# Kernel tuning notes

Measured on AMD Instinct MI355X. Metric: run time of the kernel, lower is better.

Reference implementation:

```python
import jax, jax.numpy as jnp
import numpy as np

TOP_K = 16
NUM_HEADS = 1
EPS = 1e-8  # torch F.cosine_similarity eps


def setup_inputs() -> dict:
    key = jax.random.key(0)
    ks = jax.random.split(key, 8)
    B, N, Dk, Dv = 64, 8192, 256, 256
    return {
        "query": jax.random.normal(ks[0], (B, Dk), jnp.float32),
        "key_memory": jax.random.normal(ks[1], (B, N, Dk), jnp.float32),
        "value_memory": jax.random.normal(ks[2], (B, N, Dv), jnp.float32),
        "iteration": jax.random.randint(ks[3], (B, 1), 0, N),
        "in_proj_w": jax.random.normal(ks[4], (3 * Dv, Dv), jnp.float32) * 0.06,
        "in_proj_b": jnp.zeros((3 * Dv,), jnp.float32),
        "out_proj_w": jax.random.normal(ks[5], (Dv, Dv), jnp.float32) * 0.06,
        "out_proj_b": jnp.zeros((Dv,), jnp.float32),
    }


def _mha(x, in_w, in_b, out_w, out_b):
    # torch nn.MultiheadAttention (batch_first, qkv same embed dim) self-attention
    B, T, E = x.shape
    H = NUM_HEADS
    hd = E // H
    qkv = x @ in_w.T + in_b                      # [B,T,3E]
    q, k, v = jnp.split(qkv, 3, axis=-1)

    def heads(t):
        return t.reshape(B, T, H, hd).transpose(0, 2, 1, 3)  # [B,H,T,hd]

    q, k, v = heads(q), heads(k), heads(v)
    scale = jnp.asarray(1.0 / np.sqrt(hd), x.dtype)
    attn = jax.nn.softmax(jnp.einsum('bhqd,bhkd->bhqk', q, k) * scale, axis=-1)
    o = jnp.einsum('bhqk,bhkd->bhqd', attn, v).transpose(0, 2, 1, 3).reshape(B, T, E)
    return o @ out_w.T + out_b


def reference(query, key_memory, value_memory, iteration,
              in_proj_w, in_proj_b, out_proj_w, out_proj_b):
    B, N, Dv = value_memory.shape
    # memory validity mask: item n is valid iff n <= iteration[b]
    mem_idx = jnp.arange(N)[None, :]                                   # [1,N]
    mask = (mem_idx <= iteration).astype(key_memory.dtype)[..., None]  # [B,N,1]
    km = key_memory * mask
    vm = value_memory * mask

    # masked cosine similarity between each memory key and the query
    num = jnp.einsum('bnd,bd->bn', km, query)                          # [B,N]
    denom = jnp.maximum(
        jnp.linalg.norm(km, axis=-1) * jnp.linalg.norm(query, axis=-1, keepdims=True),
        EPS)
    sim = num / denom                                                  # [B,N]

    topk_sim, topk_idx = jax.lax.top_k(sim, TOP_K)                     # [B,K]
    topk_vm = jnp.take_along_axis(vm, topk_idx[:, :, None], axis=1)    # [B,K,Dv]

    wv = jax.nn.softmax(topk_sim, axis=-1)[..., None]                  # [B,K,1]
    nrv = wv * topk_vm                                                 # [B,K,Dv]

    nrv = _mha(nrv, in_proj_w, in_proj_b, out_proj_w, out_proj_b)      # [B,K,Dv]

    # rows with iteration == 0 are left as zeros (scatter of computed rows)
    not_first = (iteration.reshape(-1) > 0).astype(nrv.dtype)[:, None, None]
    nrv = nrv * not_first
    return nrv.sum(axis=1)                                             # [B,Dv]
```

## Files before the change

kernel.cpp:

```cpp
#include <hip/hip_runtime.h>
#include <hip/hip_bf16.h>
#include <math.h>

#define B_   64
#define N_   8192
#define D_   256
#define K_   16
#define NCH_ 32
#define CPB_ 2048
#define EPS_ 1e-8f
#define NEG_ -3.4e38f

static const size_t CANDV_OFF = 0;
static const size_t CANDI_OFF = 131072;
static const size_t QKV_OFF   = 262144;

__global__ void __launch_bounds__(256)
simtopk_kernel(const float* __restrict__ q, const float* __restrict__ km,
               const int* __restrict__ iter,
               float* __restrict__ cand_v, int* __restrict__ cand_i) {
    int b     = blockIdx.x >> 5;
    int chunk = blockIdx.x & (NCH_ - 1);
    int tid   = threadIdx.x;
    int w     = tid >> 6;
    int lane  = tid & 63;
    int g     = lane >> 4;
    int p     = lane & 15;
    int it    = iter[b];
    int r0    = (chunk << 8) + (w << 6);
    size_t cbase = ((size_t)blockIdx.x * 4 + w) * K_;

    if (r0 > it) {
        if (lane < K_) { cand_v[cbase + lane] = 0.f; cand_i[cbase + lane] = r0 + lane; }
        return;
    }

    __shared__ float svals[256];

    float4 q4[4];
    #pragma unroll
    for (int k = 0; k < 4; k++)
        q4[k] = *(const float4*)(q + (size_t)b * D_ + k * 64 + p * 4);
    float qq = 0.f;
    #pragma unroll
    for (int k = 0; k < 4; k++)
        qq += q4[k].x*q4[k].x + q4[k].y*q4[k].y + q4[k].z*q4[k].z + q4[k].w*q4[k].w;
    #pragma unroll
    for (int off = 8; off; off >>= 1) qq += __shfl_xor(qq, off);
    float qn = sqrtf(qq);

    for (int t = 0; t < 16; t++) {
        int r = r0 + (t << 2) + g;
        float s = 0.f;
        if (r <= it) {
            const float* rp = km + ((size_t)b * N_ + r) * D_;
            float dot = 0.f, sq = 0.f;
            #pragma unroll
            for (int k = 0; k < 4; k++) {
                float4 kv = *(const float4*)(rp + k * 64 + p * 4);
                dot += kv.x*q4[k].x + kv.y*q4[k].y + kv.z*q4[k].z + kv.w*q4[k].w;
                sq  += kv.x*kv.x + kv.y*kv.y + kv.z*kv.z + kv.w*kv.w;
            }
            #pragma unroll
            for (int off = 8; off; off >>= 1) {
                dot += __shfl_xor(dot, off);
                sq  += __shfl_xor(sq,  off);
            }
            s = dot / fmaxf(sqrtf(sq) * qn, EPS_);
        }
        if (p == 0) svals[(w << 6) + (t << 2) + g] = s;
    }

    float v  = svals[(w << 6) + lane];
    int  idx = r0 + lane;
    for (int sel = 0; sel < K_; sel++) {
        float bv = v; int bi = idx;
        #pragma unroll
        for (int off = 32; off; off >>= 1) {
            float ov = __shfl_xor(bv, off);
            int   oi = __shfl_xor(bi, off);
            if (ov > bv || (ov == bv && oi < bi)) { bv = ov; bi = oi; }
        }
        if (idx == bi) v = NEG_;
        if (lane == 0) { cand_v[cbase + sel] = bv; cand_i[cbase + sel] = bi; }
    }
}

__global__ void __launch_bounds__(256)
merge_qkv_kernel(const float* __restrict__ cand_v, const int* __restrict__ cand_i,
                 const float* __restrict__ vm, const int* __restrict__ iter,
                 const float* __restrict__ inw, const float* __restrict__ inb,
                 float* __restrict__ qkv) {
    int b = blockIdx.x / 3, which = blockIdx.x - b * 3;
    int tid = threadIdx.x, w = tid >> 6, lane = tid & 63;
    int it = iter[b];
    if (it == 0) return;

    float cv[8]; int ci[8];
    #pragma unroll
    for (int j = 0; j < 8; j++) {
        cv[j] = cand_v[(size_t)b * CPB_ + (j << 8) + tid];
        ci[j] = cand_i[(size_t)b * CPB_ + (j << 8) + tid];
    }

    __shared__ float rv4[4]; __shared__ int ri4[4];
    __shared__ float selv[K_]; __shared__ int seli[K_];
    __shared__ float w16[K_];
    __shared__ float xs[D_][K_];

    for (int sel = 0; sel < K_; sel++) {
        float bv = cv[0]; int bi = ci[0];
        #pragma unroll
        for (int j = 1; j < 8; j++)
            if (cv[j] > bv || (cv[j] == bv && ci[j] < bi)) { bv = cv[j]; bi = ci[j]; }
        #pragma unroll
        for (int off = 32; off; off >>= 1) {
            float ov = __shfl_xor(bv, off);
            int   oi = __shfl_xor(bi, off);
            if (ov > bv || (ov == bv && oi < bi)) { bv = ov; bi = oi; }
        }
        if (lane == 0) { rv4[w] = bv; ri4[w] = bi; }
        __syncthreads();
        float wv = rv4[0]; int wi = ri4[0];
        #pragma unroll
        for (int w2 = 1; w2 < 4; w2++)
            if (rv4[w2] > wv || (rv4[w2] == wv && ri4[w2] < wi)) { wv = rv4[w2]; wi = ri4[w2]; }
        #pragma unroll
        for (int j = 0; j < 8; j++) if (ci[j] == wi) cv[j] = NEG_;
        if (tid == 0) { selv[sel] = wv; seli[sel] = wi; }
        __syncthreads();
    }

    if (tid < K_) {
        float m = NEG_;
        for (int jj = 0; jj < K_; jj++) m = fmaxf(m, selv[jj]);
        float ssum = 0.f;
        for (int jj = 0; jj < K_; jj++) ssum += expf(selv[jj] - m);
        w16[tid] = expf(selv[tid] - m) / ssum;
    }
    __syncthreads();

    #pragma unroll
    for (int k = 0; k < K_; k++) {
        int row = seli[k];
        float val = (row <= it) ? w16[k] * vm[((size_t)b * N_ + row) * D_ + tid] : 0.f;
        xs[tid][k] = val;
    }
    __syncthreads();

    float acc[K_];
    #pragma unroll
    for (int k = 0; k < K_; k++) acc[k] = 0.f;
    const float* wrow = inw + ((size_t)(which * D_ + tid)) * D_;
    for (int d = 0; d < D_; d += 4) {
        float4 wv4 = *(const float4*)(wrow + d);
        float wk[4] = {wv4.x, wv4.y, wv4.z, wv4.w};
        #pragma unroll
        for (int dd = 0; dd < 4; dd++) {
            float wgt = wk[dd];
            float4 x0 = *(const float4*)(&xs[d + dd][0]);
            float4 x1 = *(const float4*)(&xs[d + dd][4]);
            float4 x2 = *(const float4*)(&xs[d + dd][8]);
            float4 x3 = *(const float4*)(&xs[d + dd][12]);
            acc[0]  += x0.x * wgt; acc[1]  += x0.y * wgt; acc[2]  += x0.z * wgt; acc[3]  += x0.w * wgt;
            acc[4]  += x1.x * wgt; acc[5]  += x1.y * wgt; acc[6]  += x1.z * wgt; acc[7]  += x1.w * wgt;
            acc[8]  += x2.x * wgt; acc[9]  += x2.y * wgt; acc[10] += x2.z * wgt; acc[11] += x2.w * wgt;
            acc[12] += x3.x * wgt; acc[13] += x3.y * wgt; acc[14] += x3.z * wgt; acc[15] += x3.w * wgt;
        }
    }
    float bias = inb[which * D_ + tid];
    #pragma unroll
    for (int k = 0; k < K_; k++)
        qkv[(((size_t)b * 3 + which) * K_ + k) * D_ + tid] = acc[k] + bias;
}

__global__ void __launch_bounds__(256)
final_kernel(const float* __restrict__ qkv, const int* __restrict__ iter,
             const float* __restrict__ ow, const float* __restrict__ ob,
             float* __restrict__ out) {
    int b = blockIdx.x, tid = threadIdx.x;
    int it = iter[b];
    if (it == 0) { out[(size_t)b * D_ + tid] = 0.f; return; }
    __shared__ float qs[K_][D_ + 1];
    __shared__ float ks[K_][D_ + 1];
    __shared__ float vs[K_][D_ + 1];
    __shared__ float attn[K_][K_];
    __shared__ float colsum[K_];
    __shared__ float so[D_];
    const float* base = qkv + (size_t)b * 3 * K_ * D_;
    #pragma unroll
    for (int k = 0; k < K_; k++) {
        qs[k][tid] = base[(0 * K_ + k) * D_ + tid];
        ks[k][tid] = base[(1 * K_ + k) * D_ + tid];
        vs[k][tid] = base[(2 * K_ + k) * D_ + tid];
    }
    __syncthreads();
    int i = tid >> 4, j = tid & 15;
    float s = 0.f;
    for (int d = 0; d < D_; d++) s += qs[i][d] * ks[j][d];
    attn[i][j] = s * 0.0625f;
    __syncthreads();
    if (tid < K_) {
        float m = NEG_;
        for (int jj = 0; jj < K_; jj++) m = fmaxf(m, attn[tid][jj]);
        float ssum = 0.f;
        for (int jj = 0; jj < K_; jj++) ssum += expf(attn[tid][jj] - m);
        float inv = 1.f / ssum;
        for (int jj = 0; jj < K_; jj++) attn[tid][jj] = expf(attn[tid][jj] - m) * inv;
    }
    __syncthreads();
    if (tid < K_) {
        float c = 0.f;
        for (int ii = 0; ii < K_; ii++) c += attn[ii][tid];
        colsum[tid] = c;
    }
    __syncthreads();
    float acc = 0.f;
    #pragma unroll
    for (int jj = 0; jj < K_; jj++) acc += colsum[jj] * vs[jj][tid];
    so[tid] = acc;
    __syncthreads();
    float o = 0.f;
    const float* orow = ow + (size_t)tid * D_;
    for (int e = 0; e < D_; e += 4) {
        float4 wv = *(const float4*)(orow + e);
        float4 sv = *(const float4*)(&so[e]);
        o += sv.x * wv.x + sv.y * wv.y + sv.z * wv.z + sv.w * wv.w;
    }
    out[(size_t)b * D_ + tid] = o + 16.f * ob[tid];
}

extern "C" void kernel_launch(void* const* d_in, const int* in_sizes, int n_in,
                              void* d_out, int out_size, void* d_ws, size_t ws_size,
                              hipStream_t stream) {
    const float* q   = (const float*)d_in[0];
    const float* km  = (const float*)d_in[1];
    const float* vm  = (const float*)d_in[2];
    const int*   it  = (const int*)  d_in[3];
    const float* inw = (const float*)d_in[4];
    const float* inb = (const float*)d_in[5];
    const float* ow  = (const float*)d_in[6];
    const float* ob  = (const float*)d_in[7];
    float* out = (float*)d_out;

    float* ws     = (float*)d_ws;
    float* cand_v = ws + CANDV_OFF;
    int*   cand_i = (int*)(ws + CANDI_OFF);
    float* qkv    = ws + QKV_OFF;

    simtopk_kernel<<<dim3(B_ * NCH_), dim3(256), 0, stream>>>(q, km, it, cand_v, cand_i);
    merge_qkv_kernel<<<dim3(B_ * 3), dim3(256), 0, stream>>>(cand_v, cand_i, vm, it, inw, inb, qkv);
    final_kernel<<<dim3(B_), dim3(256), 0, stream>>>(qkv, it, ow, ob, out);
}
```

Measured before the change: 128.6 us.

## Rework similarity top-k with bitonic sort and streamlined merge/projection kernels

The similarity kernel now has each wavefront handle two rows per step with clamped, branch-free loads, which adds memory-level parallelism. The 16 iterative argmax passes are replaced by a full 64-lane bitonic sort. The merge kernel does the 2048-candidate selection in a single wavefront without block barriers, folds the softmax weight into a per-row scale applied after projection, and reads value rows directly from global memory with weights held in registers, instead of staging through shared memory. The attention kernel pads its shared rows and uses float4 reads. The trade-off is that one-wave selection serializes more work, and value rows are re-read per block.

```diff
diff --git a/kernel.cpp b/kernel.cpp
--- a/kernel.cpp
+++ b/kernel.cpp
@@ -6,8 +6,6 @@
 #define N_   8192
 #define D_   256
 #define K_   16
-#define NCH_ 32
-#define CPB_ 2048
 #define EPS_ 1e-8f
 #define NEG_ -3.4e38f
 
@@ -19,71 +17,91 @@
 simtopk_kernel(const float* __restrict__ q, const float* __restrict__ km,
                const int* __restrict__ iter,
                float* __restrict__ cand_v, int* __restrict__ cand_i) {
-    int b     = blockIdx.x >> 5;
-    int chunk = blockIdx.x & (NCH_ - 1);
-    int tid   = threadIdx.x;
-    int w     = tid >> 6;
-    int lane  = tid & 63;
-    int g     = lane >> 4;
-    int p     = lane & 15;
-    int it    = iter[b];
-    int r0    = (chunk << 8) + (w << 6);
-    size_t cbase = ((size_t)blockIdx.x * 4 + w) * K_;
+    int tid  = threadIdx.x;
+    int w    = tid >> 6, lane = tid & 63;
+    int g    = lane >> 4, p = lane & 15;
+    int item = (blockIdx.x << 2) + w;
+    int b    = item >> 7;
+    int r0   = (item & 127) << 6;
+    int it   = iter[b];
+    size_t cbase = (size_t)item * K_;
 
     if (r0 > it) {
         if (lane < K_) { cand_v[cbase + lane] = 0.f; cand_i[cbase + lane] = r0 + lane; }
         return;
     }
 
-    __shared__ float svals[256];
-
     float4 q4[4];
     #pragma unroll
-    for (int k = 0; k < 4; k++)
-        q4[k] = *(const float4*)(q + (size_t)b * D_ + k * 64 + p * 4);
+    for (int kk = 0; kk < 4; kk++)
+        q4[kk] = *(const float4*)(q + (size_t)b * D_ + kk * 64 + p * 4);
     float qq = 0.f;
     #pragma unroll
-    for (int k = 0; k < 4; k++)
-        qq += q4[k].x*q4[k].x + q4[k].y*q4[k].y + q4[k].z*q4[k].z + q4[k].w*q4[k].w;
+    for (int kk = 0; kk < 4; kk++)
+        qq += q4[kk].x*q4[kk].x + q4[kk].y*q4[kk].y + q4[kk].z*q4[kk].z + q4[kk].w*q4[kk].w;
     #pragma unroll
     for (int off = 8; off; off >>= 1) qq += __shfl_xor(qq, off);
     float qn = sqrtf(qq);
 
-    for (int t = 0; t < 16; t++) {
-        int r = r0 + (t << 2) + g;
-        float s = 0.f;
-        if (r <= it) {
-            const float* rp = km + ((size_t)b * N_ + r) * D_;
-            float dot = 0.f, sq = 0.f;
-            #pragma unroll
-            for (int k = 0; k < 4; k++) {
-                float4 kv = *(const float4*)(rp + k * 64 + p * 4);
-                dot += kv.x*q4[k].x + kv.y*q4[k].y + kv.z*q4[k].z + kv.w*q4[k].w;
-                sq  += kv.x*kv.x + kv.y*kv.y + kv.z*kv.z + kv.w*kv.w;
-            }
-            #pragma unroll
-            for (int off = 8; off; off >>= 1) {
-                dot += __shfl_xor(dot, off);
-                sq  += __shfl_xor(sq,  off);
-            }
-            s = dot / fmaxf(sqrtf(sq) * qn, EPS_);
-        }
-        if (p == 0) svals[(w << 6) + (t << 2) + g] = s;
-    }
-
-    float v  = svals[(w << 6) + lane];
-    int  idx = r0 + lane;
-    for (int sel = 0; sel < K_; sel++) {
-        float bv = v; int bi = idx;
-        #pragma unroll
-        for (int off = 32; off; off >>= 1) {
-            float ov = __shfl_xor(bv, off);
-            int   oi = __shfl_xor(bi, off);
-            if (ov > bv || (ov == bv && oi < bi)) { bv = ov; bi = oi; }
-        }
-        if (idx == bi) v = NEG_;
-        if (lane == 0) { cand_v[cbase + sel] = bv; cand_i[cbase + sel] = bi; }
-    }
+    float keepv = 0.f;
+    const float* kmb = km + (size_t)b * N_ * D_;
+    for (int t = 0; t < 8; t++) {
+        int ra = r0 + (t << 3) + (g << 1);
+        int rb = ra + 1;
+        const float* pa = kmb + (size_t)min(ra, it) * D_;
+        const float* pb = kmb + (size_t)min(rb, it) * D_;
+        float4 ka0 = *(const float4*)(pa +   0 + p * 4);
+        float4 ka1 = *(const float4*)(pa +  64 + p * 4);
+        float4 ka2 = *(const float4*)(pa + 128 + p * 4);
+        float4 ka3 = *(const float4*)(pa + 192 + p * 4);
+        float4 kb0 = *(const float4*)(pb +   0 + p * 4);
+        float4 kb1 = *(const float4*)(pb +  64 + p * 4);
+        float4 kb2 = *(const float4*)(pb + 128 + p * 4);
+        float4 kb3 = *(const float4*)(pb + 192 + p * 4);
+        float dota = ka0.x*q4[0].x + ka0.y*q4[0].y + ka0.z*q4[0].z + ka0.w*q4[0].w
+                   + ka1.x*q4[1].x + ka1.y*q4[1].y + ka1.z*q4[1].z + ka1.w*q4[1].w
+                   + ka2.x*q4[2].x + ka2.y*q4[2].y + ka2.z*q4[2].z + ka2.w*q4[2].w
+                   + ka3.x*q4[3].x + ka3.y*q4[3].y + ka3.z*q4[3].z + ka3.w*q4[3].w;
+        float sqa  = ka0.x*ka0.x + ka0.y*ka0.y + ka0.z*ka0.z + ka0.w*ka0.w
+                   + ka1.x*ka1.x + ka1.y*ka1.y + ka1.z*ka1.z + ka1.w*ka1.w
+                   + ka2.x*ka2.x + ka2.y*ka2.y + ka2.z*ka2.z + ka2.w*ka2.w
+                   + ka3.x*ka3.x + ka3.y*ka3.y + ka3.z*ka3.z + ka3.w*ka3.w;
+        float dotb = kb0.x*q4[0].x + kb0.y*q4[0].y + kb0.z*q4[0].z + kb0.w*q4[0].w
+                   + kb1.x*q4[1].x + kb1.y*q4[1].y + kb1.z*q4[1].z + kb1.w*q4[1].w
+                   + kb2.x*q4[2].x + kb2.y*q4[2].y + kb2.z*q4[2].z + kb2.w*q4[2].w
+                   + kb3.x*q4[3].x + kb3.y*q4[3].y + kb3.z*q4[3].z + kb3.w*q4[3].w;
+        float sqb  = kb0.x*kb0.x + kb0.y*kb0.y + kb0.z*kb0.z + kb0.w*kb0.w
+                   + kb1.x*kb1.x + kb1.y*kb1.y + kb1.z*kb1.z + kb1.w*kb1.w
+                   + kb2.x*kb2.x + kb2.y*kb2.y + kb2.z*kb2.z + kb2.w*kb2.w
+                   + kb3.x*kb3.x + kb3.y*kb3.y + kb3.z*kb3.z + kb3.w*kb3.w;
+        #pragma unroll
+        for (int off = 8; off; off >>= 1) {
+            dota += __shfl_xor(dota, off);
+            sqa  += __shfl_xor(sqa,  off);
+            dotb += __shfl_xor(dotb, off);
+            sqb  += __shfl_xor(sqb,  off);
+        }
+        float sa = (ra <= it) ? dota / fmaxf(sqrtf(sqa) * qn, EPS_) : 0.f;
+        float sb = (rb <= it) ? dotb / fmaxf(sqrtf(sqb) * qn, EPS_) : 0.f;
+        keepv = (p == 2 * t)     ? sa : keepv;
+        keepv = (p == 2 * t + 1) ? sb : keepv;
+    }
+    int keepi = r0 + ((p >> 1) << 3) + (g << 1) + (p & 1);
+
+    #pragma unroll
+    for (int k = 2; k <= 64; k <<= 1) {
+        #pragma unroll
+        for (int j = k >> 1; j > 0; j >>= 1) {
+            float pv = __shfl_xor(keepv, j);
+            int   pi = __shfl_xor(keepi, j);
+            bool up         = ((lane & k) == 0);
+            bool is_lower   = ((lane & j) == 0);
+            bool mine_first = (keepv > pv) || (keepv == pv && keepi < pi);
+            bool take_mine  = ((is_lower == up) == mine_first);
+            if (!take_mine) { keepv = pv; keepi = pi; }
+        }
+    }
+    if (lane < K_) { cand_v[cbase + lane] = keepv; cand_i[cbase + lane] = keepi; }
 }
 
 __global__ void __launch_bounds__(256)
@@ -91,99 +109,91 @@
                  const float* __restrict__ vm, const int* __restrict__ iter,
                  const float* __restrict__ inw, const float* __restrict__ inb,
                  float* __restrict__ qkv) {
-    int b = blockIdx.x / 3, which = blockIdx.x - b * 3;
-    int tid = threadIdx.x, w = tid >> 6, lane = tid & 63;
+    int bwh = blockIdx.x;
+    int b = bwh / 3, which = bwh - b * 3;
+    int tid = threadIdx.x, lane = tid & 63;
     int it = iter[b];
     if (it == 0) return;
 
-    float cv[8]; int ci[8];
-    #pragma unroll
-    for (int j = 0; j < 8; j++) {
-        cv[j] = cand_v[(size_t)b * CPB_ + (j << 8) + tid];
-        ci[j] = cand_i[(size_t)b * CPB_ + (j << 8) + tid];
-    }
-
-    __shared__ float rv4[4]; __shared__ int ri4[4];
-    __shared__ float selv[K_]; __shared__ int seli[K_];
-    __shared__ float w16[K_];
-    __shared__ float xs[D_][K_];
-
-    for (int sel = 0; sel < K_; sel++) {
-        float bv = cv[0]; int bi = ci[0];
-        #pragma unroll
-        for (int j = 1; j < 8; j++)
-            if (cv[j] > bv || (cv[j] == bv && ci[j] < bi)) { bv = cv[j]; bi = ci[j]; }
-        #pragma unroll
-        for (int off = 32; off; off >>= 1) {
-            float ov = __shfl_xor(bv, off);
-            int   oi = __shfl_xor(bi, off);
-            if (ov > bv || (ov == bv && oi < bi)) { bv = ov; bi = oi; }
-        }
-        if (lane == 0) { rv4[w] = bv; ri4[w] = bi; }
-        __syncthreads();
-        float wv = rv4[0]; int wi = ri4[0];
-        #pragma unroll
-        for (int w2 = 1; w2 < 4; w2++)
-            if (rv4[w2] > wv || (rv4[w2] == wv && ri4[w2] < wi)) { wv = rv4[w2]; wi = ri4[w2]; }
-        #pragma unroll
-        for (int j = 0; j < 8; j++) if (ci[j] == wi) cv[j] = NEG_;
-        if (tid == 0) { selv[sel] = wv; seli[sel] = wi; }
-        __syncthreads();
-    }
-
-    if (tid < K_) {
+    __shared__ int   seli[K_];
+    __shared__ float selv[K_];
+    __shared__ float scl[K_];
+
+    if (tid < 64) {
+        float cv[32]; int ci[32];
+        #pragma unroll
+        for (int j = 0; j < 32; j++) {
+            cv[j] = cand_v[(size_t)b * 2048 + (j << 6) + lane];
+            ci[j] = cand_i[(size_t)b * 2048 + (j << 6) + lane];
+        }
+        for (int sel = 0; sel < K_; sel++) {
+            float bv = cv[0]; int bi = ci[0];
+            #pragma unroll
+            for (int j = 1; j < 32; j++)
+                if (cv[j] > bv || (cv[j] == bv && ci[j] < bi)) { bv = cv[j]; bi = ci[j]; }
+            #pragma unroll
+            for (int off = 32; off; off >>= 1) {
+                float ov = __shfl_xor(bv, off);
+                int   oi = __shfl_xor(bi, off);
+                if (ov > bv || (ov == bv && oi < bi)) { bv = ov; bi = oi; }
+            }
+            #pragma unroll
+            for (int j = 0; j < 32; j++)
+                if (ci[j] == bi) cv[j] = NEG_;
+            if (lane == 0) { selv[sel] = bv; seli[sel] = bi; }
+        }
         float m = NEG_;
+        #pragma unroll
         for (int jj = 0; jj < K_; jj++) m = fmaxf(m, selv[jj]);
         float ssum = 0.f;
+        #pragma unroll
         for (int jj = 0; jj < K_; jj++) ssum += expf(selv[jj] - m);
-        w16[tid] = expf(selv[tid] - m) / ssum;
-    }
-    __syncthreads();
-
-    #pragma unroll
-    for (int k = 0; k < K_; k++) {
-        int row = seli[k];
-        float val = (row <= it) ? w16[k] * vm[((size_t)b * N_ + row) * D_ + tid] : 0.f;
-        xs[tid][k] = val;
+        if (lane < K_) {
+            int row = seli[lane];
+            float wgt = expf(selv[lane] - m) / ssum;
+            scl[lane] = (row <= it) ? wgt : 0.f;
+        }
     }
     __syncthreads();
 
     float acc[K_];
     #pragma unroll
     for (int k = 0; k < K_; k++) acc[k] = 0.f;
-    const float* wrow = inw + ((size_t)(which * D_ + tid)) * D_;
-    for (int d = 0; d < D_; d += 4) {
-        float4 wv4 = *(const float4*)(wrow + d);
-        float wk[4] = {wv4.x, wv4.y, wv4.z, wv4.w};
-        #pragma unroll
-        for (int dd = 0; dd < 4; dd++) {
-            float wgt = wk[dd];
-            float4 x0 = *(const float4*)(&xs[d + dd][0]);
-            float4 x1 = *(const float4*)(&xs[d + dd][4]);
-            float4 x2 = *(const float4*)(&xs[d + dd][8]);
-            float4 x3 = *(const float4*)(&xs[d + dd][12]);
-            acc[0]  += x0.x * wgt; acc[1]  += x0.y * wgt; acc[2]  += x0.z * wgt; acc[3]  += x0.w * wgt;
-            acc[4]  += x1.x * wgt; acc[5]  += x1.y * wgt; acc[6]  += x1.z * wgt; acc[7]  += x1.w * wgt;
-            acc[8]  += x2.x * wgt; acc[9]  += x2.y * wgt; acc[10] += x2.z * wgt; acc[11] += x2.w * wgt;
-            acc[12] += x3.x * wgt; acc[13] += x3.y * wgt; acc[14] += x3.z * wgt; acc[15] += x3.w * wgt;
+    const float* wrow = inw + (size_t)(which * D_ + tid) * D_;
+    for (int blk = 0; blk < 4; blk++) {
+        float4 wreg[16];
+        #pragma unroll
+        for (int u = 0; u < 16; u++)
+            wreg[u] = *(const float4*)(wrow + blk * 64 + u * 4);
+        #pragma unroll
+        for (int k = 0; k < K_; k++) {
+            int row = __builtin_amdgcn_readfirstlane(seli[k]);
+            const float* vr = vm + ((size_t)b * N_ + row) * D_ + blk * 64;
+            float a = 0.f;
+            #pragma unroll
+            for (int u = 0; u < 16; u++) {
+                float4 xv = *(const float4*)(vr + u * 4);
+                a += xv.x*wreg[u].x + xv.y*wreg[u].y + xv.z*wreg[u].z + xv.w*wreg[u].w;
+            }
+            acc[k] += a;
         }
     }
     float bias = inb[which * D_ + tid];
     #pragma unroll
     for (int k = 0; k < K_; k++)
-        qkv[(((size_t)b * 3 + which) * K_ + k) * D_ + tid] = acc[k] + bias;
+        qkv[(((size_t)b * 3 + which) * K_ + k) * D_ + tid] = scl[k] * acc[k] + bias;
 }
 
 __global__ void __launch_bounds__(256)
-final_kernel(const float* __restrict__ qkv, const int* __restrict__ iter,
-             const float* __restrict__ ow, const float* __restrict__ ob,
-             float* __restrict__ out) {
+attn_out_kernel(const float* __restrict__ qkv, const int* __restrict__ iter,
+                const float* __restrict__ ow, const float* __restrict__ ob,
+                float* __restrict__ out) {
     int b = blockIdx.x, tid = threadIdx.x;
     int it = iter[b];
     if (it == 0) { out[(size_t)b * D_ + tid] = 0.f; return; }
-    __shared__ float qs[K_][D_ + 1];
-    __shared__ float ks[K_][D_ + 1];
-    __shared__ float vs[K_][D_ + 1];
+    __shared__ float qs[K_][260];
+    __shared__ float ks[K_][260];
+    __shared__ float vs[K_][260];
     __shared__ float attn[K_][K_];
     __shared__ float colsum[K_];
     __shared__ float so[D_];
@@ -197,7 +207,11 @@
     __syncthreads();
     int i = tid >> 4, j = tid & 15;
     float s = 0.f;
-    for (int d = 0; d < D_; d++) s += qs[i][d] * ks[j][d];
+    for (int d4 = 0; d4 < 64; d4++) {
+        float4 qv = *(const float4*)(&qs[i][d4 * 4]);
+        float4 kv = *(const float4*)(&ks[j][d4 * 4]);
+        s += qv.x*kv.x + qv.y*kv.y + qv.z*kv.z + qv.w*kv.w;
+    }
     attn[i][j] = s * 0.0625f;
     __syncthreads();
     if (tid < K_) {
@@ -225,7 +239,7 @@
     for (int e = 0; e < D_; e += 4) {
         float4 wv = *(const float4*)(orow + e);
         float4 sv = *(const float4*)(&so[e]);
-        o += sv.x * wv.x + sv.y * wv.y + sv.z * wv.z + sv.w * wv.w;
+        o += sv.x*wv.x + sv.y*wv.y + sv.z*wv.z + sv.w*wv.w;
     }
     out[(size_t)b * D_ + tid] = o + 16.f * ob[tid];
 }
@@ -248,7 +262,7 @@
     int*   cand_i = (int*)(ws + CANDI_OFF);
     float* qkv    = ws + QKV_OFF;
 
-    simtopk_kernel<<<dim3(B_ * NCH_), dim3(256), 0, stream>>>(q, km, it, cand_v, cand_i);
+    simtopk_kernel<<<dim3(2048), dim3(256), 0, stream>>>(q, km, it, cand_v, cand_i);
     merge_qkv_kernel<<<dim3(B_ * 3), dim3(256), 0, stream>>>(cand_v, cand_i, vm, it, inw, inb, qkv);
-    final_kernel<<<dim3(B_), dim3(256), 0, stream>>>(qkv, it, ow, ob, out);
-}
+    attn_out_kernel<<<dim3(B_), dim3(256), 0, stream>>>(qkv, it, ow, ob, out);
+}
```

New measurement: 158.4 us. 1.23x slower.
